# Optimization experiments

Measured on AMD Instinct MI355X. Metric: run time of the kernel, lower is better.

Reference implementation:

```python
import jax, jax.numpy as jnp
import numpy as np

B, C, L = 16, 384, 4096
KS, NS = 32, 6
KLEN = KS * 2 ** (NS - 1)  # 1024, must be < L
DECAY = 2.0  # multiplier = linspace(2,2,C) == 2 everywhere
EPS = 1e-5


def setup_inputs() -> dict:
    key = jax.random.key(0)
    ks = jax.random.split(key, 10)
    x = jax.random.normal(ks[0], (B, C, L), jnp.float32)
    t_cond = jax.random.normal(ks[1], (B, C // 3, L), jnp.float32)
    # SLConv params (heads=1): per-scale kernels (NS, heads=1, C, KS) and skip D (1, C)
    kernels = jax.random.normal(ks[2], (NS, 1, C, KS), jnp.float32)
    D = jax.random.normal(ks[3], (1, C), jnp.float32)
    # adaLN linear: Linear(C//3 -> 6C). Original zero-inits (identity block); use small random.
    ada_w = jax.random.normal(ks[4], (6 * C, C // 3), jnp.float32) * 0.02
    ada_b = jax.random.normal(ks[5], (6 * C,), jnp.float32) * 0.02
    # 1x1 conv MLP params (kernel_size=1 -> pointwise linear), torch Conv1d init
    lim = 1.0 / np.sqrt(C)
    w1 = jax.random.uniform(ks[6], (C, C), jnp.float32, -lim, lim)
    b1 = jax.random.uniform(ks[7], (C,), jnp.float32, -lim, lim)
    w2 = jax.random.uniform(ks[8], (C, C), jnp.float32, -lim, lim)
    b2 = jax.random.uniform(ks[9], (C,), jnp.float32, -lim, lim)
    return {"x": x, "t_cond": t_cond, "kernels": kernels, "D": D,
            "ada_w": ada_w, "ada_b": ada_b, "w1": w1, "b1": b1, "w2": w2, "b2": b2}


def _channel_ln(x):
    # LayerNorm over channel dim of (B, C, L), no affine (torch eps=1e-5, biased var)
    mu = jnp.mean(x, axis=1, keepdims=True)
    var = jnp.var(x, axis=1, keepdims=True)
    return (x - mu) / jnp.sqrt(var + EPS)


def _slconv(x, kernels, D):
    # Build multi-scale kernel: nearest interp by 2**max(0,i-1), decay multiplier 2**(NS-i-1)
    klist = [jnp.repeat(kernels[i], 2 ** max(0, i - 1), axis=-1) * (DECAY ** (NS - i - 1))
             for i in range(NS)]
    k = jnp.concatenate(klist, axis=-1)  # (1, C, KLEN)
    # first-forward kernel_norm initialization: detached norm
    knorm = jax.lax.stop_gradient(jnp.linalg.norm(k, axis=-1, keepdims=True))
    k = k / knorm
    # FFT conv; SLConv hardcodes padding_mode='constant' -> factor 2
    n = 2 * L
    k_f = jnp.fft.rfft(k, n=n)          # (1, C, n//2+1)
    u_f = jnp.fft.rfft(x, n=n)          # (B, C, n//2+1)
    y_f = u_f[:, None] * k_f[None]      # einsum 'bhl,chl->bchl', heads c=1 -> (B,1,C,n//2+1)
    y = jnp.fft.irfft(y_f, n=n)         # (B, 1, C, 2L)
    ss = KLEN // 2
    y = y[..., ss:ss + L]
    y = y.reshape(B, C, L)              # 'b c h l -> b (h c) l' with heads c=1
    # skip term: einsum('bhl,ch->bchl', x, D) with c=1 collapses to x * D[0]
    return y + x * D[0][None, :, None]


def reference(x, t_cond, kernels, D, ada_w, ada_b, w1, b1, w2, b2):
    y = _channel_ln(x)
    # adaLN: SiLU then Linear over channel dim of t_cond
    t = jax.nn.silu(jnp.swapaxes(t_cond, 1, 2))              # (B, L, C//3)
    temp = jnp.swapaxes(t @ ada_w.T + ada_b, 1, 2)           # (B, 6C, L)
    shift_tm, scale_tm, gate_tm, shift_cm, scale_cm, gate_cm = jnp.split(temp, 6, axis=1)
    y = y * (1.0 + scale_tm) + shift_tm                      # modulate
    y = _slconv(y, kernels, D)
    x = x + gate_tm * y
    y = _channel_ln(x)
    y = y * (1.0 + scale_cm) + shift_cm
    h = jax.nn.gelu(jnp.einsum('oc,bcl->bol', w1, y) + b1[None, :, None], approximate=False)
    m = jnp.einsum('oc,bcl->bol', w2, h) + b2[None, :, None]
    return x + gate_cm * m
```

## Files before the change

### kernel.cpp

```cpp
#include <hip/hip_runtime.h>
#include <cstddef>
#include <cstdint>


namespace {

constexpr int B_  = 16;
constexpr int C_  = 384;
constexpr int L_  = 4096;
constexpr int KADA = 128;
constexpr int KS  = 32;
constexpr int NB  = 6 * 33;
constexpr float EPS_ = 1e-5f;
constexpr int RSA = 136;

typedef unsigned short u16;
typedef __attribute__((ext_vector_type(8))) short bf16x8;
typedef __attribute__((ext_vector_type(4))) float f32x4;
typedef __attribute__((ext_vector_type(4))) float f4;

__device__ __forceinline__ float4 ld4(const float* p) { return *reinterpret_cast<const float4*>(p); }
__device__ __forceinline__ void st4(float* p, float4 v) { *reinterpret_cast<float4*>(p) = v; }
__device__ __forceinline__ float siluf(float z) { return z / (1.f + expf(-z)); }
__device__ __forceinline__ float geluf(float z) { return 0.5f * z * (1.f + erff(z * 0.70710678118654752f)); }
__device__ __forceinline__ u16 f2b(float x) {
  union { float f; uint32_t u; } a; a.f = x;
  const uint32_t u = a.u;
  return (u16)((u + 0x7fffu + ((u >> 16) & 1u)) >> 16);
}
__device__ __forceinline__ bf16x8 ldb8(const u16* p) { return *reinterpret_cast<const bf16x8*>(p); }
__device__ __forceinline__ void stb8(u16* p, bf16x8 v) { *reinterpret_cast<bf16x8*>(p) = v; }

__global__ __launch_bounds__(64) void k_kw(const float* __restrict__ kern, float* __restrict__ wb) {
  const int c = blockIdx.x;
  const int t = threadIdx.x;
  constexpr float SC[6] = {32.f, 16.f, 8.f, 4.f, 2.f, 1.f};
  constexpr int REP[6] = {1, 1, 2, 4, 8, 16};
  float part = 0.f;
  for (int idx = t; idx < 192; idx += 64) {
    const int i = idx >> 5, r = idx & 31;
    const float v = kern[(i * C_ + c) * KS + r] * SC[i];
    part += v * v * (float)REP[i];
  }
  for (int m = 1; m < 64; m <<= 1) part += __shfl_xor(part, m);
  const float rinv = 1.f / sqrtf(part);
  for (int jj = t; jj < NB; jj += 64) {
    const int i = jj / 33, r = jj - 33 * i;
    const float sc = SC[i] * rinv;
    float bwv;
    if (r == 0) bwv = kern[(i * C_ + c) * KS + 0] * sc;
    else if (r == 32) bwv = -kern[(i * C_ + c) * KS + 31] * sc;
    else bwv = (kern[(i * C_ + c) * KS + r] - kern[(i * C_ + c) * KS + r - 1]) * sc;
    wb[c * NB + jj] = bwv;
  }
}

__global__ __launch_bounds__(256) void k_wcvt(const float* __restrict__ src, u16* __restrict__ dst) {
  const size_t i = ((size_t)blockIdx.x * 256 + threadIdx.x) * 8;
  const float4 a = ld4(src + i);
  const float4 b = ld4(src + i + 4);
  bf16x8 v;
  v[0] = (short)f2b(a.x); v[1] = (short)f2b(a.y); v[2] = (short)f2b(a.z); v[3] = (short)f2b(a.w);
  v[4] = (short)f2b(b.x); v[5] = (short)f2b(b.y); v[6] = (short)f2b(b.z); v[7] = (short)f2b(b.w);
  stb8(dst + i, v);
}

__global__ __launch_bounds__(256) void k_tsilu(const float* __restrict__ in, u16* __restrict__ out) {
  __shared__ float T[64][65];
  const int t = threadIdx.x;
  const int lb = blockIdx.x * 64;
  const int kb = blockIdx.y * 64;
  const int b  = blockIdx.z;
  const float* src = in + ((size_t)b * KADA + kb) * L_ + lb;
  const int ll = t & 63;
  const int kq = t >> 6;
  #pragma unroll
  for (int j = 0; j < 16; ++j) {
    const int k = kq * 16 + j;
    T[k][ll] = siluf(src[(size_t)k * L_ + ll]);
  }
  __syncthreads();
  const int g = t & 7;
  #pragma unroll
  for (int j = 0; j < 2; ++j) {
    const int l = (t >> 3) + 32 * j;
    bf16x8 v;
    #pragma unroll
    for (int i = 0; i < 8; ++i) v[i] = (short)f2b(T[8 * g + i][l]);
    stb8(out + ((size_t)b * L_ + lb + l) * KADA + kb + 8 * g, v);
  }
}

__global__ __launch_bounds__(256) void k_mv4(const float* __restrict__ x,
                                             float* __restrict__ mu, float* __restrict__ rs) {
  const int g4 = blockIdx.x * 256 + threadIdx.x;
  const int b = g4 >> 10;
  const int l = (g4 & 1023) * 4;
  const float* p = x + (size_t)b * C_ * L_ + l;
  f4 s = {0.f, 0.f, 0.f, 0.f}, ss = {0.f, 0.f, 0.f, 0.f};
  #pragma unroll 4
  for (int c = 0; c < C_; ++c) {
    const f4 v = *reinterpret_cast<const f4*>(p + (size_t)c * L_);
    s += v; ss += v * v;
  }
  f4 m4, r4;
  #pragma unroll
  for (int e = 0; e < 4; ++e) {
    const float m = s[e] * (1.f / (float)C_);
    const float var = ss[e] * (1.f / (float)C_) - m * m;
    m4[e] = m;
    r4[e] = 1.f / sqrtf(var + EPS_);
  }
  *reinterpret_cast<f4*>(mu + (size_t)b * L_ + l) = m4;
  *reinterpret_cast<f4*>(rs + (size_t)b * L_ + l) = r4;
}

template <int KD, int NBOP>
__device__ __forceinline__ void gemm_core3(const u16* __restrict__ Ab,
                                           const u16* __restrict__ B0b,
                                           const u16* __restrict__ B1b,
                                           u16* As, u16* Bs,
                                           f32x4 (&acc0)[4][4], f32x4 (&acc1)[4][4]) {
  constexpr int WC = (NBOP == 2) ? 2 : 4;
  const int tid = threadIdx.x;
  const int lane = tid & 63;
  const int wid = tid >> 6;
  const int wl = (wid & 1) * 64;
  const int wc = (wid >> 1) * ((NBOP == 2) ? 32 : 64);
  const int frow = lane & 15;
  const int fk8 = (lane >> 4) * 8;
  const int rr = tid >> 4;
  const int c8 = (tid & 15) * 8;

  for (int kc = 0; kc < KD; kc += 128) {
    __syncthreads();
    #pragma unroll
    for (int j = 0; j < 8; ++j)
      stb8(As + (j * 16 + rr) * RSA + c8, ldb8(Ab + (size_t)(j * 16 + rr) * KD + kc + c8));
    #pragma unroll
    for (int j = 0; j < 4; ++j)
      stb8(Bs + (j * 16 + rr) * RSA + c8, ldb8(B0b + (size_t)(j * 16 + rr) * KD + kc + c8));
    #pragma unroll
    for (int j = 0; j < 4; ++j)
      stb8(Bs + ((j + 4) * 16 + rr) * RSA + c8, ldb8(B1b + (size_t)(j * 16 + rr) * KD + kc + c8));
    __syncthreads();
    #pragma unroll
    for (int ks = 0; ks < 128; ks += 32) {
      bf16x8 af[4], b0f[WC], b1f[WC];
      #pragma unroll
      for (int fi = 0; fi < 4; ++fi)
        af[fi] = ldb8(As + (wl + fi * 16 + frow) * RSA + ks + fk8);
      #pragma unroll
      for (int fj = 0; fj < WC; ++fj) {
        b0f[fj] = ldb8(Bs + (wc + fj * 16 + frow) * RSA + ks + fk8);
        if constexpr (NBOP == 2)
          b1f[fj] = ldb8(Bs + (64 + wc + fj * 16 + frow) * RSA + ks + fk8);
      }
      #pragma unroll
      for (int fi = 0; fi < 4; ++fi)
        #pragma unroll
        for (int fj = 0; fj < WC; ++fj) {
          acc0[fi][fj] = __builtin_amdgcn_mfma_f32_16x16x32_bf16(af[fi], b0f[fj], acc0[fi][fj], 0, 0, 0);
          if constexpr (NBOP == 2)
            acc1[fi][fj] = __builtin_amdgcn_mfma_f32_16x16x32_bf16(af[fi], b1f[fj], acc1[fi][fj], 0, 0, 0);
        }
    }
  }
}

template <int MODE>
__global__ __launch_bounds__(256) void k_adagemm(const u16* __restrict__ AWB,
                                                 const float* __restrict__ ada_b,
                                                 const u16* __restrict__ STT,
                                                 const float* __restrict__ src,
                                                 const float* __restrict__ aux,
                                                 const float* __restrict__ mu,
                                                 const float* __restrict__ rs,
                                                 float* __restrict__ dstf,
                                                 u16* __restrict__ dstb,
                                                 int base0, int base1) {
  __shared__ u16 As[128 * RSA];
  __shared__ u16 Bs[128 * RSA];
  const int lb = blockIdx.x * 128;
  const int b  = blockIdx.z;
  f32x4 acc0[4][4] = {};
  f32x4 acc1[4][4] = {};
  constexpr int NBOP = (MODE == 2) ? 1 : 2;
  const int cb = blockIdx.y * ((MODE == 2) ? 128 : 64);
  const u16* B0b;
  const u16* B1b;
  if constexpr (MODE == 2) {
    B0b = AWB + (size_t)(base0 + cb) * KADA;
    B1b = AWB + (size_t)(base0 + cb + 64) * KADA;
  } else {
    B0b = AWB + (size_t)(base0 + cb) * KADA;
    B1b = AWB + (size_t)(base1 + cb) * KADA;
  }
  gemm_core3<KADA, NBOP>(STT + ((size_t)b * L_ + lb) * KADA, B0b, B1b, As, Bs, acc0, acc1);

  const int lane = threadIdx.x & 63;
  const int wid = threadIdx.x >> 6;
  const int wl = (wid & 1) * 64;
  const int wc = (wid >> 1) * ((NBOP == 2) ? 32 : 64);
  const int frow = lane & 15;
  const int fq = (lane >> 4) * 4;
  constexpr int WC = (NBOP == 2) ? 2 : 4;
  #pragma unroll
  for (int fi = 0; fi < 4; ++fi) {
    const int lg = lb + wl + fi * 16 + fq;
    float4 m4, r4;
    if (MODE != 2) { m4 = ld4(mu + (size_t)b * L_ + lg); r4 = ld4(rs + (size_t)b * L_ + lg); }
    #pragma unroll
    for (int fj = 0; fj < WC; ++fj) {
      const int cg = cb + wc + fj * 16 + frow;
      const size_t n = ((size_t)b * C_ + cg) * L_ + lg;
      if (MODE == 2) {
        const float bg = ada_b[base0 + cg];
        const float4 xv = ld4(src + n);
        const float4 yv = ld4(aux + n);
        float4 o;
        o.x = xv.x + (acc0[fi][fj][0] + bg) * yv.x;
        o.y = xv.y + (acc0[fi][fj][1] + bg) * yv.y;
        o.z = xv.z + (acc0[fi][fj][2] + bg) * yv.z;
        o.w = xv.w + (acc0[fi][fj][3] + bg) * yv.w;
        st4(dstf + n, o);
      } else {
        const float bsh = ada_b[base0 + cg];
        const float bsc = ada_b[base1 + cg];
        const float4 xv = ld4(src + n);
        float o[4];
        o[0] = (xv.x - m4.x) * r4.x * (1.f + acc1[fi][fj][0] + bsc) + acc0[fi][fj][0] + bsh;
        o[1] = (xv.y - m4.y) * r4.y * (1.f + acc1[fi][fj][1] + bsc) + acc0[fi][fj][1] + bsh;
        o[2] = (xv.z - m4.z) * r4.z * (1.f + acc1[fi][fj][2] + bsc) + acc0[fi][fj][2] + bsh;
        o[3] = (xv.w - m4.w) * r4.w * (1.f + acc1[fi][fj][3] + bsc) + acc0[fi][fj][3] + bsh;
        if (MODE == 0) {
          st4(dstf + n, float4{o[0], o[1], o[2], o[3]});
        } else {
          u16* d = dstb + ((size_t)b * L_ + lg) * C_ + cg;
          #pragma unroll
          for (int i = 0; i < 4; ++i) d[(size_t)i * C_] = f2b(o[i]);
        }
      }
    }
  }
}

__global__ __launch_bounds__(256) void k_mlp1(const u16* __restrict__ Y3T,
                                              const u16* __restrict__ W1B,
                                              const float* __restrict__ b1,
                                              u16* __restrict__ HT) {
  __shared__ u16 As[128 * RSA];
  __shared__ u16 Bs[128 * RSA];
  const int lb = blockIdx.x * 128;
  const int cb = blockIdx.y * 128;
  const int b  = blockIdx.z;
  f32x4 acc0[4][4] = {};
  f32x4 accd[4][4];
  gemm_core3<C_, 1>(Y3T + ((size_t)b * L_ + lb) * C_,
                    W1B + (size_t)cb * C_, W1B + (size_t)(cb + 64) * C_,
                    As, Bs, acc0, accd);
  const int lane = threadIdx.x & 63;
  const int wid = threadIdx.x >> 6;
  const int wl = (wid & 1) * 64;
  const int wc = (wid >> 1) * 64;
  const int frow = lane & 15;
  const int fq = (lane >> 4) * 4;
  #pragma unroll
  for (int fi = 0; fi < 4; ++fi) {
    const int lg = lb + wl + fi * 16 + fq;
    #pragma unroll
    for (int fj = 0; fj < 4; ++fj) {
      const int hg = cb + wc + fj * 16 + frow;
      const float bo = b1[hg];
      u16* d = HT + ((size_t)b * L_ + lg) * C_ + hg;
      #pragma unroll
      for (int i = 0; i < 4; ++i) d[(size_t)i * C_] = f2b(geluf(acc0[fi][fj][i] + bo));
    }
  }
}

__global__ __launch_bounds__(256) void k_final(const u16* __restrict__ HT,
                                               const u16* __restrict__ W2B,
                                               const float* __restrict__ b2,
                                               const u16* __restrict__ AWB,
                                               const float* __restrict__ ada_b,
                                               const u16* __restrict__ STT,
                                               float* __restrict__ out,
                                               int gbase) {
  __shared__ u16 As[128 * RSA];
  __shared__ u16 Bs[128 * RSA];
  const int lb = blockIdx.x * 128;
  const int cb = blockIdx.y * 128;
  const int b  = blockIdx.z;
  f32x4 accM[4][4] = {};
  f32x4 accG[4][4] = {};
  f32x4 accd[4][4];
  gemm_core3<C_, 1>(HT + ((size_t)b * L_ + lb) * C_,
                    W2B + (size_t)cb * C_, W2B + (size_t)(cb + 64) * C_,
                    As, Bs, accM, accd);
  gemm_core3<KADA, 1>(STT + ((size_t)b * L_ + lb) * KADA,
                      AWB + (size_t)(gbase + cb) * KADA,
                      AWB + (size_t)(gbase + cb + 64) * KADA,
                      As, Bs, accG, accd);
  const int lane = threadIdx.x & 63;
  const int wid = threadIdx.x >> 6;
  const int wl = (wid & 1) * 64;
  const int wc = (wid >> 1) * 64;
  const int frow = lane & 15;
  const int fq = (lane >> 4) * 4;
  #pragma unroll
  for (int fi = 0; fi < 4; ++fi) {
    const int lg = lb + wl + fi * 16 + fq;
    #pragma unroll
    for (int fj = 0; fj < 4; ++fj) {
      const int cg = cb + wc + fj * 16 + frow;
      const float bo = b2[cg];
      const float bg = ada_b[gbase + cg];
      const size_t n = ((size_t)b * C_ + cg) * L_ + lg;
      const float4 xv = ld4(out + n);
      float4 o;
      o.x = xv.x + (accG[fi][fj][0] + bg) * (accM[fi][fj][0] + bo);
      o.y = xv.y + (accG[fi][fj][1] + bg) * (accM[fi][fj][1] + bo);
      o.z = xv.z + (accG[fi][fj][2] + bg) * (accM[fi][fj][2] + bo);
      o.w = xv.w + (accG[fi][fj][3] + bg) * (accM[fi][fj][3] + bo);
      st4(out + n, o);
    }
  }
}

__device__ __forceinline__ int sidx(int i) { return i + (i >> 4); }

__global__ __launch_bounds__(256) void k_scan(float* __restrict__ data) {
  __shared__ float s[4352];
  __shared__ float aux[256];
  const int tid = threadIdx.x;
  float* row = data + (size_t)blockIdx.x * L_;
  #pragma unroll
  for (int j = 0; j < 16; ++j) s[sidx(j * 256 + tid)] = row[j * 256 + tid];
  __syncthreads();
  const int base = tid * 16;
  float run = 0.f, loc[16];
  #pragma unroll
  for (int j = 0; j < 16; ++j) { run += s[sidx(base + j)]; loc[j] = run; }
  aux[tid] = run;
  __syncthreads();
  for (int off = 1; off < 256; off <<= 1) {
    const float t = (tid >= off) ? aux[tid - off] : 0.f;
    __syncthreads();
    aux[tid] += t;
    __syncthreads();
  }
  const float excl = tid ? aux[tid - 1] : 0.f;
  #pragma unroll
  for (int j = 0; j < 16; ++j) s[sidx(base + j)] = loc[j] + excl;
  __syncthreads();
  #pragma unroll
  for (int j = 0; j < 16; ++j) row[j * 256 + tid] = s[sidx(j * 256 + tid)];
}

__device__ __forceinline__ int swz(int q) { return q ^ ((q >> 3) & 7); }

__device__ __forceinline__ float wf5(const f4& W0, const f4& W1, const f4& W2,
                                     const f4& W3, const f4& W4, int j) {
  return j < 4 ? W0[j & 3] : j < 8 ? W1[j & 3] : j < 12 ? W2[j & 3]
       : j < 16 ? W3[j & 3] : W4[j & 3];
}
__device__ __forceinline__ float wf4(const f4& W0, const f4& W1, const f4& W2,
                                     const f4& W3, int j) {
  return j < 4 ? W0[j & 3] : j < 8 ? W1[j & 3] : j < 12 ? W2[j & 3] : W3[j & 3];
}

__global__ __launch_bounds__(256) void k_conv(float* __restrict__ A,
                                              const float* __restrict__ wb,
                                              const float* __restrict__ Dv) {
  __shared__ f4 Q4s[1280];
  const int tid = threadIdx.x;
  const int c = blockIdx.x % C_;
  float* row = A + (size_t)blockIdx.x * L_;
  if (tid < 128) Q4s[swz(tid)] = f4{0.f, 0.f, 0.f, 0.f};
  #pragma unroll
  for (int j = 0; j < 4; ++j) {
    const int q = 128 + j * 256 + tid;
    Q4s[swz(q)] = *reinterpret_cast<const f4*>(row + 4 * (j * 256 + tid));
  }
  __syncthreads();
  const float last = Q4s[swz(1151)][3];
  if (tid < 128) Q4s[swz(1152 + tid)] = f4{last, last, last, last};
  __syncthreads();

  const float* wrow = wb + c * NB;
  const int qb = 256 + 4 * tid;
  float acc[16];
  #pragma unroll
  for (int i = 0; i < 16; ++i) acc[i] = 0.f;

  #pragma unroll
  for (int s = 0; s < 2; ++s) {
    const int wbase = s * 33;
    const int q0 = qb - 1 - 8 * s;
    float w[33];
    #pragma unroll
    for (int r = 0; r < 33; ++r) w[r] = wrow[wbase + r];
    f4 W0 = Q4s[swz(q0)],     W1 = Q4s[swz(q0 + 1)], W2 = Q4s[swz(q0 + 2)],
       W3 = Q4s[swz(q0 + 3)], W4 = Q4s[swz(q0 + 4)];
    #pragma unroll
    for (int g = 0; g < 9; ++g) {
      #pragma unroll
      for (int d = 0; d < 4; ++d) {
        if (g < 8 || d == 0) {
          #pragma unroll
          for (int i = 0; i < 16; ++i)
            acc[i] += w[4 * g + d] * wf5(W0, W1, W2, W3, W4, i + 4 - d);
        }
      }
      if (g < 8) { W4 = W3; W3 = W2; W2 = W1; W1 = W0; W0 = Q4s[swz(q0 - 1 - g)]; }
    }
  }
  {
    const int q0 = qb - 17;
    float w[33];
    #pragma unroll
    for (int r = 0; r < 33; ++r) w[r] = wrow[66 + r];
    f4 W0 = Q4s[swz(q0)],     W1 = Q4s[swz(q0 + 1)], W2 = Q4s[swz(q0 + 2)],
       W3 = Q4s[swz(q0 + 3)], W4 = Q4s[swz(q0 + 4)];
    #pragma unroll
    for (int h = 0; h < 17; ++h) {
      #pragma unroll
      for (int i = 0; i < 16; ++i)
        acc[i] += w[2 * h] * wf5(W0, W1, W2, W3, W4, i + 4);
      if (h < 16) {
        #pragma unroll
        for (int i = 0; i < 16; ++i)
          acc[i] += w[2 * h + 1] * wf5(W0, W1, W2, W3, W4, i + 2);
        W4 = W3; W3 = W2; W2 = W1; W1 = W0; W0 = Q4s[swz(q0 - 1 - h)];
      }
    }
  }
  {
    const int low0 = qb - 32;
    float w[33];
    #pragma unroll
    for (int r = 0; r < 33; ++r) w[r] = wrow[99 + r];
    f4 W0 = Q4s[swz(low0)],     W1 = Q4s[swz(low0 + 1)],
       W2 = Q4s[swz(low0 + 2)], W3 = Q4s[swz(low0 + 3)];
    #pragma unroll
    for (int r = 0; r < 33; ++r) {
      #pragma unroll
      for (int i = 0; i < 16; ++i) acc[i] += w[r] * wf4(W0, W1, W2, W3, i);
      if (r < 32) { W3 = W2; W2 = W1; W1 = W0; W0 = Q4s[swz(low0 - 1 - r)]; }
    }
  }
  {
    const int low0 = qb - 64;
    float w[33];
    #pragma unroll
    for (int r = 0; r < 33; ++r) w[r] = wrow[132 + r];
    f4 W0 = Q4s[swz(low0)],     W1 = Q4s[swz(low0 + 1)],
       W2 = Q4s[swz(low0 + 2)], W3 = Q4s[swz(low0 + 3)];
    #pragma unroll
    for (int r = 0; r < 33; ++r) {
      #pragma unroll
      for (int i = 0; i < 16; ++i) acc[i] += w[r] * wf4(W0, W1, W2, W3, i);
      if (r < 32) {
        W3 = W1; W2 = W0;
        W0 = Q4s[swz(low0 - 2 * r - 2)];
        W1 = Q4s[swz(low0 - 2 * r - 1)];
      }
    }
  }
  {
    float w[33];
    #pragma unroll
    for (int r = 0; r < 33; ++r) w[r] = wrow[165 + r];
    #pragma unroll
    for (int r = 0; r < 33; ++r) {
      const int lo = qb - 128 - 4 * r;
      const f4 W0 = Q4s[swz(lo)],     W1 = Q4s[swz(lo + 1)],
               W2 = Q4s[swz(lo + 2)], W3 = Q4s[swz(lo + 3)];
      #pragma unroll
      for (int i = 0; i < 16; ++i) acc[i] += w[r] * wf4(W0, W1, W2, W3, i);
    }
  }

  const float Dc = Dv[c];
  const int qe = 128 + 4 * tid;
  const f4 E0 = Q4s[swz(qe - 1)], E1 = Q4s[swz(qe)],     E2 = Q4s[swz(qe + 1)],
           E3 = Q4s[swz(qe + 2)], E4 = Q4s[swz(qe + 3)];
  float pm[17];
  #pragma unroll
  for (int j = 0; j < 17; ++j) pm[j] = wf5(E0, E1, E2, E3, E4, j + 3);
  #pragma unroll
  for (int a = 0; a < 4; ++a) {
    f4 o;
    #pragma unroll
    for (int e = 0; e < 4; ++e)
      o[e] = acc[4 * a + e] + (pm[4 * a + e + 1] - pm[4 * a + e]) * Dc;
    *reinterpret_cast<f4*>(row + 16 * tid + 4 * a) = o;
  }
}

}

extern "C" void kernel_launch(void* const* d_in, const int* in_sizes, int n_in,
                              void* d_out, int out_size, void* d_ws, size_t ws_size,
                              hipStream_t stream) {
  const float* x      = (const float*)d_in[0];
  const float* t_cond = (const float*)d_in[1];
  const float* kern   = (const float*)d_in[2];
  const float* Dv     = (const float*)d_in[3];
  const float* ada_w  = (const float*)d_in[4];
  const float* ada_b  = (const float*)d_in[5];
  const float* w1     = (const float*)d_in[6];
  const float* b1     = (const float*)d_in[7];
  const float* w2     = (const float*)d_in[8];
  const float* b2     = (const float*)d_in[9];
  float* out = (float*)d_out;

  float* wsf = (float*)d_ws;
  float* A  = wsf;
  float* MV = A + (size_t)B_ * C_ * L_;
  float* WB = MV + 4 * (size_t)B_ * L_;
  u16* AWB = (u16*)(WB + (size_t)C_ * NB);
  u16* W1B = AWB + (size_t)6 * C_ * KADA;
  u16* W2B = W1B + (size_t)C_ * C_;
  u16* STT = W2B + (size_t)C_ * C_;
  u16* Y3T = STT + (size_t)B_ * L_ * KADA;
  u16* HT  = Y3T + (size_t)B_ * L_ * C_;
  float* mu1 = MV;
  float* rs1 = MV + (size_t)B_ * L_;
  float* mu2 = MV + 2 * (size_t)B_ * L_;
  float* rs2 = MV + 3 * (size_t)B_ * L_;

  (void)in_sizes; (void)n_in; (void)out_size; (void)ws_size;

  const dim3 gg2(L_ / 128, 6, B_);
  const dim3 gg3(L_ / 128, 3, B_);

  k_kw<<<C_, 64, 0, stream>>>(kern, WB);
  k_wcvt<<<(6 * C_ * KADA) / 2048, 256, 0, stream>>>(ada_w, AWB);
  k_wcvt<<<(C_ * C_) / 2048, 256, 0, stream>>>(w1, W1B);
  k_wcvt<<<(C_ * C_) / 2048, 256, 0, stream>>>(w2, W2B);
  k_tsilu<<<dim3(L_ / 64, KADA / 64, B_), 256, 0, stream>>>(t_cond, STT);

  k_mv4<<<(B_ * L_ / 4) / 256, 256, 0, stream>>>(x, mu1, rs1);
  k_adagemm<0><<<gg2, 256, 0, stream>>>(AWB, ada_b, STT, x, nullptr, mu1, rs1, A, nullptr, 0, C_);
  k_scan<<<B_ * C_, 256, 0, stream>>>(A);
  k_conv<<<B_ * C_, 256, 0, stream>>>(A, WB, Dv);
  k_adagemm<2><<<gg3, 256, 0, stream>>>(AWB, ada_b, STT, x, A, nullptr, nullptr, out, nullptr, 2 * C_, 0);
  k_mv4<<<(B_ * L_ / 4) / 256, 256, 0, stream>>>(out, mu2, rs2);
  k_adagemm<1><<<gg2, 256, 0, stream>>>(AWB, ada_b, STT, out, nullptr, mu2, rs2, nullptr, Y3T, 3 * C_, 4 * C_);
  k_mlp1<<<gg3, 256, 0, stream>>>(Y3T, W1B, b1, HT);
  k_final<<<gg3, 256, 0, stream>>>(HT, W2B, b2, AWB, ada_b, STT, out, 5 * C_);
}
```

Baseline: 593.1 us.

## Fuse prefix scan and gated residual into the conv kernel, gate stored as bf16

The separate prefix-scan kernel and the conv kernel become one kernel. It loads the modulated row, does the per-thread and block scan in registers and shared memory, then runs the conv. The gated residual x + gate*y, previously applied by the MODE 2 adagemm, is now done in the conv epilogue. MODE 2 now only writes the gate as bf16 into a reused buffer. This removes a full fp32 read/write pass over the activations and one launch, at the cost of rounding the gate to bf16.

Measured after the change: 647.6 us. 1.09x slower.

```diff
diff --git a/kernel.cpp b/kernel.cpp
--- a/kernel.cpp
+++ b/kernel.cpp
@@ -27,6 +27,9 @@
   union { float f; uint32_t u; } a; a.f = x;
   const uint32_t u = a.u;
   return (u16)((u + 0x7fffu + ((u >> 16) & 1u)) >> 16);
+}
+__device__ __forceinline__ float b2f(u16 h) {
+  union { uint32_t u; float f; } a; a.u = ((uint32_t)h) << 16; return a.f;
 }
 __device__ __forceinline__ bf16x8 ldb8(const u16* p) { return *reinterpret_cast<const bf16x8*>(p); }
 __device__ __forceinline__ void stb8(u16* p, bf16x8 v) { *reinterpret_cast<bf16x8*>(p) = v; }
@@ -173,7 +176,6 @@
                                                  const float* __restrict__ ada_b,
                                                  const u16* __restrict__ STT,
                                                  const float* __restrict__ src,
-                                                 const float* __restrict__ aux,
                                                  const float* __restrict__ mu,
                                                  const float* __restrict__ rs,
                                                  float* __restrict__ dstf,
@@ -216,14 +218,14 @@
       const size_t n = ((size_t)b * C_ + cg) * L_ + lg;
       if (MODE == 2) {
         const float bg = ada_b[base0 + cg];
-        const float4 xv = ld4(src + n);
-        const float4 yv = ld4(aux + n);
-        float4 o;
-        o.x = xv.x + (acc0[fi][fj][0] + bg) * yv.x;
-        o.y = xv.y + (acc0[fi][fj][1] + bg) * yv.y;
-        o.z = xv.z + (acc0[fi][fj][2] + bg) * yv.z;
-        o.w = xv.w + (acc0[fi][fj][3] + bg) * yv.w;
-        st4(dstf + n, o);
+        const u16 h0 = f2b(acc0[fi][fj][0] + bg);
+        const u16 h1 = f2b(acc0[fi][fj][1] + bg);
+        const u16 h2 = f2b(acc0[fi][fj][2] + bg);
+        const u16 h3 = f2b(acc0[fi][fj][3] + bg);
+        uint2 pk;
+        pk.x = (uint32_t)h0 | ((uint32_t)h1 << 16);
+        pk.y = (uint32_t)h2 | ((uint32_t)h3 << 16);
+        *reinterpret_cast<uint2*>(dstb + n) = pk;
       } else {
         const float bsh = ada_b[base0 + cg];
         const float bsc = ada_b[base1 + cg];
@@ -328,21 +330,44 @@
   }
 }
 
-__device__ __forceinline__ int sidx(int i) { return i + (i >> 4); }
-
-__global__ __launch_bounds__(256) void k_scan(float* __restrict__ data) {
-  __shared__ float s[4352];
+__device__ __forceinline__ int swz(int q) { return q ^ ((q >> 3) & 7); }
+
+__device__ __forceinline__ float wf5(const f4& W0, const f4& W1, const f4& W2,
+                                     const f4& W3, const f4& W4, int j) {
+  return j < 4 ? W0[j & 3] : j < 8 ? W1[j & 3] : j < 12 ? W2[j & 3]
+       : j < 16 ? W3[j & 3] : W4[j & 3];
+}
+__device__ __forceinline__ float wf4(const f4& W0, const f4& W1, const f4& W2,
+                                     const f4& W3, int j) {
+  return j < 4 ? W0[j & 3] : j < 8 ? W1[j & 3] : j < 12 ? W2[j & 3] : W3[j & 3];
+}
+
+__global__ __launch_bounds__(256) void k_convfused(const float* __restrict__ Ymod,
+                                                   const float* __restrict__ x,
+                                                   const u16* __restrict__ G,
+                                                   const float* __restrict__ wb,
+                                                   const float* __restrict__ Dv,
+                                                   float* __restrict__ out) {
+  __shared__ f4 Q4s[1280];
   __shared__ float aux[256];
   const int tid = threadIdx.x;
-  float* row = data + (size_t)blockIdx.x * L_;
-  #pragma unroll
-  for (int j = 0; j < 16; ++j) s[sidx(j * 256 + tid)] = row[j * 256 + tid];
-  __syncthreads();
-  const int base = tid * 16;
-  float run = 0.f, loc[16];
-  #pragma unroll
-  for (int j = 0; j < 16; ++j) { run += s[sidx(base + j)]; loc[j] = run; }
-  aux[tid] = run;
+  const int c = blockIdx.x % C_;
+  const size_t rowoff = (size_t)blockIdx.x * L_;
+
+  f4 v[4];
+  {
+    const float* yrow = Ymod + rowoff;
+    #pragma unroll
+    for (int j = 0; j < 4; ++j)
+      v[j] = *reinterpret_cast<const f4*>(yrow + 16 * tid + 4 * j);
+    float run = 0.f;
+    #pragma unroll
+    for (int j = 0; j < 4; ++j) {
+      v[j][0] += run; v[j][1] += v[j][0]; v[j][2] += v[j][1]; v[j][3] += v[j][2];
+      run = v[j][3];
+    }
+    aux[tid] = run;
+  }
   __syncthreads();
   for (int off = 1; off < 256; off <<= 1) {
     const float t = (tid >= off) ? aux[tid - off] : 0.f;
@@ -351,41 +376,16 @@
     __syncthreads();
   }
   const float excl = tid ? aux[tid - 1] : 0.f;
-  #pragma unroll
-  for (int j = 0; j < 16; ++j) s[sidx(base + j)] = loc[j] + excl;
-  __syncthreads();
-  #pragma unroll
-  for (int j = 0; j < 16; ++j) row[j * 256 + tid] = s[sidx(j * 256 + tid)];
-}
-
-__device__ __forceinline__ int swz(int q) { return q ^ ((q >> 3) & 7); }
-
-__device__ __forceinline__ float wf5(const f4& W0, const f4& W1, const f4& W2,
-                                     const f4& W3, const f4& W4, int j) {
-  return j < 4 ? W0[j & 3] : j < 8 ? W1[j & 3] : j < 12 ? W2[j & 3]
-       : j < 16 ? W3[j & 3] : W4[j & 3];
-}
-__device__ __forceinline__ float wf4(const f4& W0, const f4& W1, const f4& W2,
-                                     const f4& W3, int j) {
-  return j < 4 ? W0[j & 3] : j < 8 ? W1[j & 3] : j < 12 ? W2[j & 3] : W3[j & 3];
-}
-
-__global__ __launch_bounds__(256) void k_conv(float* __restrict__ A,
-                                              const float* __restrict__ wb,
-                                              const float* __restrict__ Dv) {
-  __shared__ f4 Q4s[1280];
-  const int tid = threadIdx.x;
-  const int c = blockIdx.x % C_;
-  float* row = A + (size_t)blockIdx.x * L_;
-  if (tid < 128) Q4s[swz(tid)] = f4{0.f, 0.f, 0.f, 0.f};
+  const float total = aux[255];
   #pragma unroll
   for (int j = 0; j < 4; ++j) {
-    const int q = 128 + j * 256 + tid;
-    Q4s[swz(q)] = *reinterpret_cast<const f4*>(row + 4 * (j * 256 + tid));
-  }
-  __syncthreads();
-  const float last = Q4s[swz(1151)][3];
-  if (tid < 128) Q4s[swz(1152 + tid)] = f4{last, last, last, last};
+    v[j][0] += excl; v[j][1] += excl; v[j][2] += excl; v[j][3] += excl;
+    Q4s[swz(128 + 4 * tid + j)] = v[j];
+  }
+  if (tid < 128) {
+    Q4s[swz(tid)] = f4{0.f, 0.f, 0.f, 0.f};
+    Q4s[swz(1152 + tid)] = f4{total, total, total, total};
+  }
   __syncthreads();
 
   const float* wrow = wb + c * NB;
@@ -483,19 +483,25 @@
   }
 
   const float Dc = Dv[c];
-  const int qe = 128 + 4 * tid;
-  const f4 E0 = Q4s[swz(qe - 1)], E1 = Q4s[swz(qe)],     E2 = Q4s[swz(qe + 1)],
-           E3 = Q4s[swz(qe + 2)], E4 = Q4s[swz(qe + 3)];
-  float pm[17];
-  #pragma unroll
-  for (int j = 0; j < 17; ++j) pm[j] = wf5(E0, E1, E2, E3, E4, j + 3);
+  const float* xrow = x + rowoff + 16 * tid;
+  const u16* grow = G + rowoff + 16 * tid;
+  float* orow = out + rowoff + 16 * tid;
+  const bf16x8 g0 = ldb8(grow);
+  const bf16x8 g1 = ldb8(grow + 8);
+  float pprev = excl;
   #pragma unroll
   for (int a = 0; a < 4; ++a) {
+    const f4 xv = *reinterpret_cast<const f4*>(xrow + 4 * a);
     f4 o;
     #pragma unroll
-    for (int e = 0; e < 4; ++e)
-      o[e] = acc[4 * a + e] + (pm[4 * a + e + 1] - pm[4 * a + e]) * Dc;
-    *reinterpret_cast<f4*>(row + 16 * tid + 4 * a) = o;
+    for (int e = 0; e < 4; ++e) {
+      const int i = 4 * a + e;
+      const float y2 = acc[i] + (v[a][e] - pprev) * Dc;
+      const float gv = b2f((u16)(i < 8 ? g0[i] : g1[i - 8]));
+      o[e] = xv[e] + gv * y2;
+      pprev = v[a][e];
+    }
+    *reinterpret_cast<f4*>(orow + 4 * a) = o;
   }
 }
 
@@ -526,6 +532,7 @@
   u16* STT = W2B + (size_t)C_ * C_;
   u16* Y3T = STT + (size_t)B_ * L_ * KADA;
   u16* HT  = Y3T + (size_t)B_ * L_ * C_;
+  u16* G   = Y3T;
   float* mu1 = MV;
   float* rs1 = MV + (size_t)B_ * L_;
   float* mu2 = MV + 2 * (size_t)B_ * L_;
@@ -543,12 +550,11 @@
   k_tsilu<<<dim3(L_ / 64, KADA / 64, B_), 256, 0, stream>>>(t_cond, STT);
 
   k_mv4<<<(B_ * L_ / 4) / 256, 256, 0, stream>>>(x, mu1, rs1);
-  k_adagemm<0><<<gg2, 256, 0, stream>>>(AWB, ada_b, STT, x, nullptr, mu1, rs1, A, nullptr, 0, C_);
-  k_scan<<<B_ * C_, 256, 0, stream>>>(A);
-  k_conv<<<B_ * C_, 256, 0, stream>>>(A, WB, Dv);
-  k_adagemm<2><<<gg3, 256, 0, stream>>>(AWB, ada_b, STT, x, A, nullptr, nullptr, out, nullptr, 2 * C_, 0);
+  k_adagemm<0><<<gg2, 256, 0, stream>>>(AWB, ada_b, STT, x, mu1, rs1, A, nullptr, 0, C_);
+  k_adagemm<2><<<gg3, 256, 0, stream>>>(AWB, ada_b, STT, nullptr, nullptr, nullptr, nullptr, G, 2 * C_, 0);
+  k_convfused<<<B_ * C_, 256, 0, stream>>>(A, x, G, WB, Dv, out);
   k_mv4<<<(B_ * L_ / 4) / 256, 256, 0, stream>>>(out, mu2, rs2);
-  k_adagemm<1><<<gg2, 256, 0, stream>>>(AWB, ada_b, STT, out, nullptr, mu2, rs2, nullptr, Y3T, 3 * C_, 4 * C_);
+  k_adagemm<1><<<gg2, 256, 0, stream>>>(AWB, ada_b, STT, out, mu2, rs2, nullptr, Y3T, 3 * C_, 4 * C_);
   k_mlp1<<<gg3, 256, 0, stream>>>(Y3T, W1B, b1, HT);
   k_final<<<gg3, 256, 0, stream>>>(HT, W2B, b2, AWB, ada_b, STT, out, 5 * C_);
 }
```
